# Performance work log

Measured on AMD Instinct MI355X. Metric: run time of the kernel, lower is better.

## Reference

```python
import jax, jax.numpy as jnp
import numpy as np

D_MODEL = 768; N_LAYER = 4; D_STATE = 64; D_CONV = 4; EXPAND = 2; HEADDIM = 64
D_INNER = EXPAND * D_MODEL          # 1536
NHEADS = D_INNER // HEADDIM         # 24
CONV_DIM = D_INNER + 2 * D_STATE    # 1664
D_IN_PROJ = 2 * D_INNER + 2 * D_STATE + NHEADS  # 3224
VOCAB = 50257; EPS = 1e-5


def _ln(x, w, b):
    m = x.mean(-1, keepdims=True)
    v = ((x - m) ** 2).mean(-1, keepdims=True)
    return (x - m) * jax.lax.rsqrt(v + EPS) * w + b


def _silu(x):
    return x * jax.nn.sigmoid(x)


def _mamba2(x, W_in, conv_w, conv_b, dt_bias, A_log, Dp, rms_w, W_out):
    # x: [B, L, d_model]
    Bsz, L, _ = x.shape
    zxbcdt = x @ W_in.T                                   # [B,L,D_IN_PROJ]
    z = zxbcdt[..., :D_INNER]
    xBC = zxbcdt[..., D_INNER:D_INNER + CONV_DIM]
    dt = zxbcdt[..., D_INNER + CONV_DIM:]                 # [B,L,H]
    # causal depthwise conv over time
    xc = jnp.transpose(xBC, (0, 2, 1))                    # [B,C,L]
    xc = jax.lax.conv_general_dilated(
        xc, conv_w[:, None, :], (1,), [(D_CONV - 1, 0)],
        dimension_numbers=('NCH', 'OIH', 'NCH'), feature_group_count=CONV_DIM)
    xBC = _silu(jnp.transpose(xc, (0, 2, 1)) + conv_b)
    xh = xBC[..., :D_INNER].reshape(Bsz, L, NHEADS, HEADDIM)
    Bc = xBC[..., D_INNER:D_INNER + D_STATE]              # [B,L,N]
    Cc = xBC[..., D_INNER + D_STATE:]                     # [B,L,N]
    dt = jax.nn.softplus(dt + dt_bias)                    # [B,L,H]
    dA = jnp.exp(dt * (-jnp.exp(A_log)))                  # [B,L,H]

    def step(h, inp):
        dA_t, dt_t, x_t, B_t, C_t = inp
        h = dA_t[:, :, None, None] * h + (dt_t[:, :, None] * x_t)[..., None] * B_t[:, None, None, :]
        return h, jnp.einsum('bhpn,bn->bhp', h, C_t)

    tm = lambda a: jnp.moveaxis(a, 1, 0)  # time-major
    h0 = jnp.zeros((Bsz, NHEADS, HEADDIM, D_STATE), x.dtype)
    _, y = jax.lax.scan(step, h0, (tm(dA), tm(dt), tm(xh), tm(Bc), tm(Cc)))
    y = jnp.moveaxis(y, 0, 1) + Dp[:, None] * xh          # [B,L,H,P]
    y = y.reshape(Bsz, L, D_INNER) * _silu(z)             # gate
    y = y * jax.lax.rsqrt((y * y).mean(-1, keepdims=True) + EPS) * rms_w
    return y @ W_out.T


def setup_inputs() -> dict:
    key = jax.random.key(0)
    ks = jax.random.split(key, 16)
    B, L = 1, 1024
    idx = jax.random.randint(ks[0], (B, L), 0, VOCAB)
    targets = jax.random.randint(ks[1], (B, L), 0, VOCAB)
    s = 0.02
    emb = jax.random.normal(ks[2], (VOCAB, D_MODEL), jnp.float32) * s
    ln_w = jnp.ones((N_LAYER, D_MODEL)); ln_b = jnp.zeros((N_LAYER, D_MODEL))
    W_in = jax.random.normal(ks[3], (N_LAYER, D_IN_PROJ, D_MODEL), jnp.float32) * s
    conv_w = jax.random.normal(ks[4], (N_LAYER, CONV_DIM, D_CONV), jnp.float32) * 0.1
    conv_b = jnp.zeros((N_LAYER, CONV_DIM))
    dt_bias = jnp.log(jnp.expm1(jax.random.uniform(ks[5], (N_LAYER, NHEADS), minval=0.001, maxval=0.1)))
    A_log = jnp.log(jax.random.uniform(ks[6], (N_LAYER, NHEADS), minval=1.0, maxval=16.0))
    Dp = jnp.ones((N_LAYER, NHEADS))
    rms_w = jnp.ones((N_LAYER, D_INNER))
    W_out = jax.random.normal(ks[7], (N_LAYER, D_MODEL, D_INNER), jnp.float32) * s
    lnf_w = jnp.ones((D_MODEL,)); lnf_b = jnp.zeros((D_MODEL,))
    return {"idx": idx, "targets": targets, "emb": emb, "ln_w": ln_w, "ln_b": ln_b,
            "W_in": W_in, "conv_w": conv_w, "conv_b": conv_b, "dt_bias": dt_bias,
            "A_log": A_log, "Dp": Dp, "rms_w": rms_w, "W_out": W_out,
            "lnf_w": lnf_w, "lnf_b": lnf_b}


def reference(idx, targets, emb, ln_w, ln_b, W_in, conv_w, conv_b, dt_bias,
              A_log, Dp, rms_w, W_out, lnf_w, lnf_b):
    x = emb[idx]                                          # [B,L,D]
    for i in range(N_LAYER):
        x = x + _mamba2(_ln(x, ln_w[i], ln_b[i]), W_in[i], conv_w[i], conv_b[i],
                        dt_bias[i], A_log[i], Dp[i], rms_w[i], W_out[i])
    x = _ln(x, lnf_w, lnf_b)
    logits = x @ emb.T                                    # tied head
    logp = jax.nn.log_softmax(logits, axis=-1)
    loss = -jnp.take_along_axis(logp, targets[..., None], axis=-1).mean()
    return logits, loss
```

## Files before the change

### kernel.cpp

```cpp
#include <hip/hip_runtime.h>
#include <hip/hip_bf16.h>
#include <math.h>

#define SL     1024
#define DMODEL 768
#define NLAYER 4
#define NSTATE 64
#define HEADDIM 64
#define DINNER 1536
#define NHEADS 24
#define CONVDIM 1664
#define DINPROJ 3224
#define VOCABN 50257

typedef __attribute__((ext_vector_type(8))) short short8;
typedef __attribute__((ext_vector_type(4))) short short4v;
typedef __attribute__((ext_vector_type(4))) float f32x4;

__device__ __forceinline__ short f2bf(float f) {
    unsigned int u = __builtin_bit_cast(unsigned int, f);
    u += 0x7fffu + ((u >> 16) & 1u);
    return (short)(u >> 16);
}

#define AS1 __attribute__((address_space(1)))
#define AS3 __attribute__((address_space(3)))
__device__ __forceinline__ void gl2lds16(const void* g, void* l) {
    __builtin_amdgcn_global_load_lds((const AS1 unsigned int*)g,
                                     (AS3 unsigned int*)(unsigned int)(uintptr_t)l,
                                     16, 0, 0);
}

template <int CTRL>
__device__ __forceinline__ float dppadd(float x) {
    int v = __builtin_amdgcn_update_dpp(0, __builtin_bit_cast(int, x), CTRL, 0xf, 0xf, true);
    return x + __builtin_bit_cast(float, v);
}

__global__ void cvt_k(const float* __restrict__ s, short* __restrict__ d, int n) {
    int i = (blockIdx.x * 256 + threadIdx.x) * 4;
    if (i >= n) return;
    float4 v = *(const float4*)(s + i);
    short4v o;
    o.x = f2bf(v.x); o.y = f2bf(v.y); o.z = f2bf(v.z); o.w = f2bf(v.w);
    *(short4v*)(d + i) = o;
}

__global__ void embed_k(const int* __restrict__ idx, const float* __restrict__ emb,
                        float* __restrict__ x) {
    int d = blockIdx.x * 256 + threadIdx.x;
    int t = blockIdx.y;
    x[t * DMODEL + d] = emb[(size_t)idx[t] * DMODEL + d];
}

__global__ void ln_k(const float* __restrict__ x, const float* __restrict__ w,
                     const float* __restrict__ b, short* __restrict__ out) {
    int row = blockIdx.x, t = threadIdx.x;
    const float* xr = x + row * DMODEL;
    float v0 = xr[t], v1 = xr[t + 256], v2 = xr[t + 512];
    float s = v0 + v1 + v2;
    float q = v0 * v0 + v1 * v1 + v2 * v2;
    __shared__ float sa[4], sb[4];
    for (int off = 32; off; off >>= 1) { s += __shfl_down(s, off); q += __shfl_down(q, off); }
    if (!(t & 63)) { sa[t >> 6] = s; sb[t >> 6] = q; }
    __syncthreads();
    s = sa[0] + sa[1] + sa[2] + sa[3];
    q = sb[0] + sb[1] + sb[2] + sb[3];
    float mean = s * (1.f / DMODEL);
    float var  = q * (1.f / DMODEL) - mean * mean;
    float rs = rsqrtf(var + 1e-5f);
    out[row * DMODEL + t      ] = f2bf((v0 - mean) * rs * w[t      ] + b[t      ]);
    out[row * DMODEL + t + 256] = f2bf((v1 - mean) * rs * w[t + 256] + b[t + 256]);
    out[row * DMODEL + t + 512] = f2bf((v2 - mean) * rs * w[t + 512] + b[t + 512]);
}

__global__ __launch_bounds__(512) void gemm_bb_k(const short* __restrict__ A,
                                                 const short* __restrict__ B,
                                                 float* __restrict__ C,
                                                 float2* __restrict__ P,
                                                 int N, int K, int addflag) {
    __shared__ __align__(16) short As[2][16384];
    __shared__ __align__(16) short Bs[2][16384];
    const int t = threadIdx.x;
    const int lane = t & 63, wv = t >> 6;

    const int nwg = gridDim.x;
    int bid = blockIdx.x;
    int qq = nwg >> 3, rr = nwg & 7;
    int xcd = bid & 7, ii = bid >> 3;
    int v = (xcd < rr ? xcd * (qq + 1) : rr * (qq + 1) + (xcd - rr) * qq) + ii;
    const int m0 = (v & 3) * 256;
    const int n0 = (v >> 2) * 256;

    const int wm = (wv >> 2) * 128, wn = (wv & 3) * 64;
    const int q4 = lane >> 4, l16 = lane & 15;

    f32x4 zero4 = {0.f, 0.f, 0.f, 0.f};
    f32x4 acc[8][4];
#pragma unroll
    for (int i = 0; i < 8; i++)
#pragma unroll
        for (int j = 0; j < 4; j++) acc[i][j] = zero4;

    auto stageA = [&](int buf, int kh, int k0) {
#pragma unroll
        for (int i = 0; i < 2; i++) {
            int g = i * 512 + t;
            int q = g >> 8, r = g & 255;
            gl2lds16(A + (size_t)(m0 + r) * K + k0 + kh * 32 + q * 8,
                     &As[buf][kh * 8192 + g * 8]);
        }
    };
    auto stageB = [&](int buf, int kh, int k0) {
#pragma unroll
        for (int i = 0; i < 2; i++) {
            int g = i * 512 + t;
            int q = g >> 8, r = g & 255;
            int gr = n0 + r; if (gr > N - 1) gr = N - 1;
            gl2lds16(B + (size_t)gr * K + k0 + kh * 32 + q * 8,
                     &Bs[buf][kh * 8192 + g * 8]);
        }
    };

    const int NT = K >> 6;
    stageA(0, 0, 0); stageB(0, 0, 0); stageA(0, 1, 0); stageB(0, 1, 0);
    asm volatile("s_waitcnt vmcnt(4)" ::: "memory");
    __builtin_amdgcn_s_barrier();

    for (int tt = 0; tt < NT; tt++) {
        const int cur = tt & 1;
        const bool pf = (tt + 1 < NT);
        const int k1 = (tt + 1) << 6;
        const short* Ac = &As[cur][0];
        const short* Bc = &Bs[cur][0];

        short8 bfk[4];
        {
            short8 af[4];
#pragma unroll
            for (int nt = 0; nt < 4; nt++)
                bfk[nt] = *(const short8*)(Bc + q4 * 2048 + (wn + nt * 16 + l16) * 8);
#pragma unroll
            for (int mt = 0; mt < 4; mt++)
                af[mt] = *(const short8*)(Ac + q4 * 2048 + (wm + mt * 16 + l16) * 8);
            if (pf) stageA(cur ^ 1, 0, k1);
            __builtin_amdgcn_s_barrier();
            __builtin_amdgcn_s_setprio(1);
#pragma unroll
            for (int mt = 0; mt < 4; mt++)
#pragma unroll
                for (int nt = 0; nt < 4; nt++)
                    acc[mt][nt] = __builtin_amdgcn_mfma_f32_16x16x32_bf16(af[mt], bfk[nt], acc[mt][nt], 0, 0, 0);
            __builtin_amdgcn_s_setprio(0);
            __builtin_amdgcn_s_barrier();
        }
        {
            short8 af[4];
#pragma unroll
            for (int mt = 0; mt < 4; mt++)
                af[mt] = *(const short8*)(Ac + q4 * 2048 + (wm + (mt + 4) * 16 + l16) * 8);
            if (pf) stageB(cur ^ 1, 0, k1);
            __builtin_amdgcn_s_barrier();
            __builtin_amdgcn_s_setprio(1);
#pragma unroll
            for (int mt = 0; mt < 4; mt++)
#pragma unroll
                for (int nt = 0; nt < 4; nt++)
                    acc[mt + 4][nt] = __builtin_amdgcn_mfma_f32_16x16x32_bf16(af[mt], bfk[nt], acc[mt + 4][nt], 0, 0, 0);
            __builtin_amdgcn_s_setprio(0);
            if (pf) asm volatile("s_waitcnt vmcnt(4)" ::: "memory");
            else    asm volatile("s_waitcnt vmcnt(0)" ::: "memory");
            __builtin_amdgcn_s_barrier();
        }
        {
            short8 af[4];
#pragma unroll
            for (int nt = 0; nt < 4; nt++)
                bfk[nt] = *(const short8*)(Bc + 8192 + q4 * 2048 + (wn + nt * 16 + l16) * 8);
#pragma unroll
            for (int mt = 0; mt < 4; mt++)
                af[mt] = *(const short8*)(Ac + 8192 + q4 * 2048 + (wm + mt * 16 + l16) * 8);
            if (pf) stageA(cur ^ 1, 1, k1);
            __builtin_amdgcn_s_barrier();
            __builtin_amdgcn_s_setprio(1);
#pragma unroll
            for (int mt = 0; mt < 4; mt++)
#pragma unroll
                for (int nt = 0; nt < 4; nt++)
                    acc[mt][nt] = __builtin_amdgcn_mfma_f32_16x16x32_bf16(af[mt], bfk[nt], acc[mt][nt], 0, 0, 0);
            __builtin_amdgcn_s_setprio(0);
            __builtin_amdgcn_s_barrier();
        }
        {
            short8 af[4];
#pragma unroll
            for (int mt = 0; mt < 4; mt++)
                af[mt] = *(const short8*)(Ac + 8192 + q4 * 2048 + (wm + (mt + 4) * 16 + l16) * 8);
            if (pf) stageB(cur ^ 1, 1, k1);
            __builtin_amdgcn_s_barrier();
            __builtin_amdgcn_s_setprio(1);
#pragma unroll
            for (int mt = 0; mt < 4; mt++)
#pragma unroll
                for (int nt = 0; nt < 4; nt++)
                    acc[mt + 4][nt] = __builtin_amdgcn_mfma_f32_16x16x32_bf16(af[mt], bfk[nt], acc[mt + 4][nt], 0, 0, 0);
            __builtin_amdgcn_s_setprio(0);
            if (pf) asm volatile("s_waitcnt vmcnt(4)" ::: "memory");
            else    asm volatile("s_waitcnt vmcnt(0)" ::: "memory");
            __builtin_amdgcn_s_barrier();
        }
    }

#pragma unroll
    for (int mt = 0; mt < 8; mt++) {
        int row = m0 + wm + mt * 16 + q4 * 4;
#pragma unroll
        for (int nt = 0; nt < 4; nt++) {
            int col = n0 + wn + nt * 16 + l16;
            if (col < N) {
#pragma unroll
                for (int r = 0; r < 4; r++) {
                    size_t o = (size_t)(row + r) * N + col;
                    float val = acc[mt][nt][r];
                    if (addflag) C[o] += val; else C[o] = val;
                }
            }
        }
    }

    float2* lds_ms = (float2*)&As[0][0];
    const int nw = wv & 3;
#pragma unroll
    for (int mt = 0; mt < 8; mt++) {
#pragma unroll
        for (int r = 0; r < 4; r++) {
            float m = -3.0e38f;
#pragma unroll
            for (int nt = 0; nt < 4; nt++) {
                int col = n0 + wn + nt * 16 + l16;
                if (col < N) m = fmaxf(m, acc[mt][nt][r]);
            }
#pragma unroll
            for (int off = 1; off < 16; off <<= 1)
                m = fmaxf(m, __shfl_xor(m, off));
            float s = 0.f;
#pragma unroll
            for (int nt = 0; nt < 4; nt++) {
                int col = n0 + wn + nt * 16 + l16;
                if (col < N) s += __expf(acc[mt][nt][r] - m);
            }
#pragma unroll
            for (int off = 1; off < 16; off <<= 1)
                s += __shfl_xor(s, off);
            if (l16 == 0)
                lds_ms[(wm + mt * 16 + q4 * 4 + r) * 5 + nw] = make_float2(m, s);
        }
    }
    __syncthreads();
    if (t < 256) {
        float m = -3.0e38f, s = 0.f;
#pragma unroll
        for (int w = 0; w < 4; w++) {
            float2 p = lds_ms[t * 5 + w];
            float nm = fmaxf(m, p.x);
            s = s * __expf(m - nm) + p.y * __expf(p.x - nm);
            m = nm;
        }
        P[(size_t)(v >> 2) * 1024 + (m0 + t)] = make_float2(m, s);
    }
}

__global__ __launch_bounds__(256) void gemm64_k(const short* __restrict__ A,
                                                const short* __restrict__ B,
                                                float* __restrict__ C,
                                                int N, int K, int addflag, int nMB) {
    __shared__ __align__(16) short As[2][4096];
    __shared__ __align__(16) short Bs[2][4096];
    const int t = threadIdx.x;
    const int lane = t & 63, wv = t >> 6;

    const int nwg = gridDim.x;
    int bid = blockIdx.x;
    int qq = nwg >> 3, rr = nwg & 7;
    int xcd = bid & 7, ii = bid >> 3;
    int v = (xcd < rr ? xcd * (qq + 1) : rr * (qq + 1) + (xcd - rr) * qq) + ii;
    const int m0 = (v % nMB) * 64, n0 = (v / nMB) * 64;

    const int wm = (wv >> 1) * 32, wn = (wv & 1) * 32;
    const int q4 = lane >> 4, l16 = lane & 15;

    f32x4 zero4 = {0.f, 0.f, 0.f, 0.f};
    f32x4 acc[2][2];
#pragma unroll
    for (int i = 0; i < 2; i++)
#pragma unroll
        for (int j = 0; j < 2; j++) acc[i][j] = zero4;

    auto stage = [&](int buf, int k0) {
#pragma unroll
        for (int i = 0; i < 2; i++) {
            int g = i * 256 + t;
            int q = g >> 6, r = g & 63;
            gl2lds16(A + (size_t)(m0 + r) * K + k0 + q * 8, &As[buf][g * 8]);
        }
#pragma unroll
        for (int i = 0; i < 2; i++) {
            int g = i * 256 + t;
            int q = g >> 6, r = g & 63;
            int gr = n0 + r; if (gr > N - 1) gr = N - 1;
            gl2lds16(B + (size_t)gr * K + k0 + q * 8, &Bs[buf][g * 8]);
        }
    };

    const int NT = K >> 6;
    stage(0, 0);
    for (int tt = 0; tt < NT; tt++) {
        const int cur = tt & 1;
        if (tt + 1 < NT) {
            stage(cur ^ 1, (tt + 1) << 6);
            asm volatile("s_waitcnt vmcnt(4)" ::: "memory");
        } else {
            asm volatile("s_waitcnt vmcnt(0)" ::: "memory");
        }
        __builtin_amdgcn_s_barrier();

        short8 af[2][2], bf[2][2];
#pragma unroll
        for (int kk = 0; kk < 2; kk++) {
#pragma unroll
            for (int mt = 0; mt < 2; mt++)
                af[kk][mt] = *(const short8*)(&As[cur][(kk * 4 + q4) * 512 + (wm + mt * 16 + l16) * 8]);
#pragma unroll
            for (int nt = 0; nt < 2; nt++)
                bf[kk][nt] = *(const short8*)(&Bs[cur][(kk * 4 + q4) * 512 + (wn + nt * 16 + l16) * 8]);
        }
        asm volatile("s_waitcnt lgkmcnt(0)" ::: "memory");
        __builtin_amdgcn_s_barrier();

#pragma unroll
        for (int kk = 0; kk < 2; kk++)
#pragma unroll
            for (int mt = 0; mt < 2; mt++)
#pragma unroll
                for (int nt = 0; nt < 2; nt++)
                    acc[mt][nt] = __builtin_amdgcn_mfma_f32_16x16x32_bf16(af[kk][mt], bf[kk][nt], acc[mt][nt], 0, 0, 0);
    }

#pragma unroll
    for (int mt = 0; mt < 2; mt++) {
        int row = m0 + wm + mt * 16 + (lane >> 4) * 4;
#pragma unroll
        for (int nt = 0; nt < 2; nt++) {
            int col = n0 + wn + nt * 16 + l16;
            if (col < N) {
#pragma unroll
                for (int r = 0; r < 4; r++) {
                    size_t o = (size_t)(row + r) * N + col;
                    float val = acc[mt][nt][r];
                    if (addflag) C[o] += val; else C[o] = val;
                }
            }
        }
    }
}

#define LDSK 56
__global__ __launch_bounds__(256) void gemm_bt_k(const short* __restrict__ A,
                                                 const float* __restrict__ B,
                                                 float* __restrict__ C,
                                                 int N, int K, int addflag) {
    __shared__ __align__(16) short As[128 * LDSK];
    __shared__ __align__(16) short Bs[128 * LDSK];
    const int t = threadIdx.x;
    const int lane = t & 63, wv = t >> 6;
    const int m0 = blockIdx.x * 128, n0 = blockIdx.y * 128;
    const int wm = (wv >> 1) * 64, wn = (wv & 1) * 64;
    f32x4 zero4 = {0.f, 0.f, 0.f, 0.f};
    f32x4 acc[4][4];
#pragma unroll
    for (int i = 0; i < 4; i++)
#pragma unroll
        for (int j = 0; j < 4; j++) acc[i][j] = zero4;
    for (int k0 = 0; k0 < K; k0 += 32) {
        uint4  av[2];
        float4 bv[4];
#pragma unroll
        for (int i = 0; i < 2; i++) {
            int c = i * 256 + t, row = c >> 2, kc = c & 3;
            av[i] = *(const uint4*)(A + (size_t)(m0 + row) * K + k0 + kc * 8);
        }
#pragma unroll
        for (int i = 0; i < 4; i++) {
            int c = i * 256 + t, row = c >> 3, kc = c & 7;
            int gr = n0 + row; if (gr > N - 1) gr = N - 1;
            bv[i] = *(const float4*)(B + (size_t)gr * K + k0 + kc * 4);
        }
        __syncthreads();
#pragma unroll
        for (int i = 0; i < 2; i++) {
            int c = i * 256 + t, row = c >> 2, kc = c & 3;
            *(uint4*)(As + row * LDSK + kc * 8) = av[i];
        }
#pragma unroll
        for (int i = 0; i < 4; i++) {
            int c = i * 256 + t, row = c >> 3, kc = c & 7;
            short4v sv;
            sv.x = f2bf(bv[i].x); sv.y = f2bf(bv[i].y);
            sv.z = f2bf(bv[i].z); sv.w = f2bf(bv[i].w);
            *(short4v*)(Bs + row * LDSK + kc * 4) = sv;
        }
        __syncthreads();
        short8 af[4], bf[4];
#pragma unroll
        for (int mt = 0; mt < 4; mt++)
            af[mt] = *(const short8*)(As + (wm + mt * 16 + (lane & 15)) * LDSK + (lane >> 4) * 8);
#pragma unroll
        for (int nt = 0; nt < 4; nt++)
            bf[nt] = *(const short8*)(Bs + (wn + nt * 16 + (lane & 15)) * LDSK + (lane >> 4) * 8);
#pragma unroll
        for (int mt = 0; mt < 4; mt++)
#pragma unroll
            for (int nt = 0; nt < 4; nt++)
                acc[mt][nt] = __builtin_amdgcn_mfma_f32_16x16x32_bf16(af[mt], bf[nt], acc[mt][nt], 0, 0, 0);
    }
#pragma unroll
    for (int mt = 0; mt < 4; mt++) {
        int row = m0 + wm + mt * 16 + (lane >> 4) * 4;
#pragma unroll
        for (int nt = 0; nt < 4; nt++) {
            int col = n0 + wn + nt * 16 + (lane & 15);
            if (col < N) {
#pragma unroll
                for (int r = 0; r < 4; r++) {
                    size_t o = (size_t)(row + r) * N + col;
                    float val = acc[mt][nt][r];
                    if (addflag) C[o] += val; else C[o] = val;
                }
            }
        }
    }
}

__global__ void convdt_k(const float* __restrict__ zx, const float* __restrict__ cw,
                         const float* __restrict__ cb, const float* __restrict__ dt_bias,
                         const float* __restrict__ A_log, float* __restrict__ xbc,
                         float* __restrict__ dts, float* __restrict__ dAv) {
    int c = blockIdx.x * 256 + threadIdx.x;
    int t = blockIdx.y;
    if (c < CONVDIM) {
        float acc = cb[c];
#pragma unroll
        for (int j = 0; j < 4; j++) {
            int ts = t - 3 + j;
            if (ts >= 0) acc += cw[c * 4 + j] * zx[(size_t)ts * DINPROJ + DINNER + c];
        }
        xbc[(size_t)t * CONVDIM + c] = acc / (1.f + __expf(-acc));
    } else if (c < CONVDIM + NHEADS) {
        int h = c - CONVDIM;
        float d = zx[(size_t)t * DINPROJ + 3200 + h] + dt_bias[h];
        float sp = (d > 20.f) ? d : log1pf(__expf(d));
        dts[t * NHEADS + h] = sp;
        dAv[t * NHEADS + h] = __expf(-__expf(A_log[h]) * sp);
    }
}

__global__ __launch_bounds__(128) void scan_k(const float* __restrict__ xbc,
                                              const float* __restrict__ dts,
                                              const float* __restrict__ dAv,
                                              float* __restrict__ yraw) {
    __shared__ __align__(16) float BCs[64][128];
    __shared__ __align__(16) float xs[64][8];
    __shared__ float dash[64];
    int h = blockIdx.x >> 3;
    int pbase = (blockIdx.x & 7) * 8;
    int t = threadIdx.x, lane = t & 63, wv = t >> 6;
    int pl = wv * 4 + (lane >> 4);
    int n4 = lane & 15;
    float s0 = 0.f, s1 = 0.f, s2 = 0.f, s3 = 0.f;

    for (int tc = 0; tc < 16; tc++) {
        __syncthreads();
#pragma unroll 4
        for (int it = 0; it < 16; it++) {
            int idx = it * 128 + t;
            int trow = idx >> 5, c4 = idx & 31;
            *(float4*)&BCs[trow][c4 * 4] =
                *(const float4*)(xbc + (size_t)(tc * 64 + trow) * CONVDIM + DINNER + c4 * 4);
        }
        {
            int trow = t >> 1, hf = t & 1;
            float dtv = dts[(tc * 64 + trow) * NHEADS + h];
            float4 xv = *(const float4*)(xbc + (size_t)(tc * 64 + trow) * CONVDIM
                                         + h * HEADDIM + pbase + hf * 4);
            xv.x *= dtv; xv.y *= dtv; xv.z *= dtv; xv.w *= dtv;
            *(float4*)&xs[trow][hf * 4] = xv;
        }
        if (t < 64) dash[t] = dAv[(tc * 64 + t) * NHEADS + h];
        __syncthreads();

#pragma unroll 4
        for (int tt = 0; tt < 64; tt++) {
            float4 B4 = *(const float4*)&BCs[tt][n4 * 4];
            float4 C4 = *(const float4*)&BCs[tt][64 + n4 * 4];
            float dtx = xs[tt][pl];
            float da = dash[tt];
            s0 = fmaf(da, s0, dtx * B4.x);
            s1 = fmaf(da, s1, dtx * B4.y);
            s2 = fmaf(da, s2, dtx * B4.z);
            s3 = fmaf(da, s3, dtx * B4.w);
            float part = s0 * C4.x;
            part = fmaf(s1, C4.y, part);
            part = fmaf(s2, C4.z, part);
            part = fmaf(s3, C4.w, part);
            part = dppadd<0xB1>(part);
            part = dppadd<0x4E>(part);
            part = dppadd<0x114>(part);
            part = dppadd<0x118>(part);
            if (n4 == 0)
                yraw[(size_t)(tc * 64 + tt) * DINNER + h * HEADDIM + pbase + pl] = part;
        }
    }
}

__global__ void rms_k(const float* __restrict__ yraw, const float* __restrict__ zx,
                      const float* __restrict__ xbc, const float* __restrict__ Dp,
                      const float* __restrict__ rw, short* __restrict__ yn) {
    int row = blockIdx.x, t = threadIdx.x;
    float v[6];
    float q = 0.f;
#pragma unroll
    for (int j = 0; j < 6; j++) {
        int i = t + j * 256;
        float z  = zx[(size_t)row * DINPROJ + i];
        float xh = xbc[(size_t)row * CONVDIM + i];
        float y  = yraw[(size_t)row * DINNER + i] + Dp[i >> 6] * xh;
        float val = y * (z / (1.f + __expf(-z)));
        v[j] = val;
        q += val * val;
    }
    __shared__ float sb[4];
    for (int off = 32; off; off >>= 1) q += __shfl_down(q, off);
    if (!(t & 63)) sb[t >> 6] = q;
    __syncthreads();
    q = sb[0] + sb[1] + sb[2] + sb[3];
    float rs = rsqrtf(q * (1.f / DINNER) + 1e-5f);
#pragma unroll
    for (int j = 0; j < 6; j++) {
        int i = t + j * 256;
        yn[(size_t)row * DINNER + i] = f2bf(v[j] * rs * rw[i]);
    }
}

__global__ void loss_row_k(const float* __restrict__ logits, const int* __restrict__ tg,
                           float* __restrict__ lossp) {
    int r = blockIdx.x, t = threadIdx.x;
    const float* lr = logits + (size_t)r * VOCABN;
    float m = -3.0e38f, s = 0.f;
    for (int j = t; j < VOCABN; j += 256) {
        float v = lr[j];
        if (v > m) { s = s * __expf(m - v) + 1.f; m = v; }
        else s += __expf(v - m);
    }
    for (int off = 32; off; off >>= 1) {
        float mo = __shfl_down(m, off), so = __shfl_down(s, off);
        float nm = fmaxf(m, mo);
        s = s * __expf(m - nm) + so * __expf(mo - nm);
        m = nm;
    }
    __shared__ float sm[4], ss[4];
    if (!(t & 63)) { sm[t >> 6] = m; ss[t >> 6] = s; }
    __syncthreads();
    if (t == 0) {
        m = sm[0]; s = ss[0];
        for (int w = 1; w < 4; w++) {
            float nm = fmaxf(m, sm[w]);
            s = s * __expf(m - nm) + ss[w] * __expf(sm[w] - nm);
            m = nm;
        }
        lossp[r] = (m + logf(s)) - lr[tg[r]];
    }
}

__global__ void loss_fin2_k(const float2* __restrict__ P, const float* __restrict__ logits,
                            const int* __restrict__ tg, float* __restrict__ lossp) {
    int r = blockIdx.x * 256 + threadIdx.x;
    float m = -3.0e38f, s = 0.f;
    for (int p = 0; p < 197; p++) {
        float2 q = P[(size_t)p * 1024 + r];
        float nm = fmaxf(m, q.x);
        s = s * __expf(m - nm) + q.y * __expf(q.x - nm);
        m = nm;
    }
    lossp[r] = (m + logf(s)) - logits[(size_t)r * VOCABN + tg[r]];
}

__global__ void loss_fin_k(const float* __restrict__ lossp, float* __restrict__ out) {
    int t = threadIdx.x;
    float s = lossp[t] + lossp[t + 256] + lossp[t + 512] + lossp[t + 768];
    for (int off = 32; off; off >>= 1) s += __shfl_down(s, off);
    __shared__ float sb[4];
    if (!(t & 63)) sb[t >> 6] = s;
    __syncthreads();
    if (t == 0) out[(size_t)SL * VOCABN] = (sb[0] + sb[1] + sb[2] + sb[3]) * (1.f / SL);
}

extern "C" void kernel_launch(void* const* d_in, const int* in_sizes, int n_in,
                              void* d_out, int out_size, void* d_ws, size_t ws_size,
                              hipStream_t stream) {
    const int*   idx     = (const int*)d_in[0];
    const int*   targets = (const int*)d_in[1];
    const float* emb     = (const float*)d_in[2];
    const float* ln_w    = (const float*)d_in[3];
    const float* ln_b    = (const float*)d_in[4];
    const float* W_in    = (const float*)d_in[5];
    const float* conv_w  = (const float*)d_in[6];
    const float* conv_b  = (const float*)d_in[7];
    const float* dt_bias = (const float*)d_in[8];
    const float* A_log   = (const float*)d_in[9];
    const float* Dp      = (const float*)d_in[10];
    const float* rms_w   = (const float*)d_in[11];
    const float* W_out   = (const float*)d_in[12];
    const float* lnf_w   = (const float*)d_in[13];
    const float* lnf_b   = (const float*)d_in[14];

    char* ws = (char*)d_ws;
    float* x     = (float*)(ws + 0);
    short* xn    = (short*)(ws + 3145728);
    float* zx    = (float*)(ws + 4718592);
    float* xbc   = (float*)(ws + 17924096);
    float* dts   = (float*)(ws + 24739840);
    float* dAv   = (float*)(ws + 24838144);
    float* yraw  = (float*)(ws + 24936448);
    short* yn    = (short*)(ws + 31227904);
    float* lossp = (float*)(ws + 34373632);
    short* wInb  = (short*)(ws + 34377728);
    short* wOutb = (short*)(ws + 54183936);
    short* embb  = (short*)(ws + 63621120);
    float2* pms  = (float2*)(ws + 4718592);
    float* logits = (float*)d_out;

    const bool big = ws_size >= 140815872ull;

    if (big) {
        int nWin  = NLAYER * DINPROJ * DMODEL;
        int nWout = NLAYER * DMODEL * DINNER;
        int nEmb  = VOCABN * DMODEL;
        cvt_k<<<(nWin / 4 + 255) / 256, 256, 0, stream>>>(W_in, wInb, nWin);
        cvt_k<<<(nWout / 4 + 255) / 256, 256, 0, stream>>>(W_out, wOutb, nWout);
        cvt_k<<<(nEmb / 4 + 255) / 256, 256, 0, stream>>>(emb, embb, nEmb);
    }

    embed_k<<<dim3(3, SL), 256, 0, stream>>>(idx, emb, x);
    for (int l = 0; l < NLAYER; l++) {
        ln_k<<<SL, 256, 0, stream>>>(x, ln_w + l * DMODEL, ln_b + l * DMODEL, xn);
        if (big)
            gemm64_k<<<816, 256, 0, stream>>>(xn, wInb + (size_t)l * DINPROJ * DMODEL,
                                              zx, DINPROJ, DMODEL, 0, 16);
        else
            gemm_bt_k<<<dim3(8, 26), 256, 0, stream>>>(xn, W_in + (size_t)l * DINPROJ * DMODEL,
                                                       zx, DINPROJ, DMODEL, 0);
        convdt_k<<<dim3(7, SL), 256, 0, stream>>>(zx, conv_w + l * CONVDIM * 4,
                                                  conv_b + l * CONVDIM,
                                                  dt_bias + l * NHEADS, A_log + l * NHEADS,
                                                  xbc, dts, dAv);
        scan_k<<<192, 128, 0, stream>>>(xbc, dts, dAv, yraw);
        rms_k<<<SL, 256, 0, stream>>>(yraw, zx, xbc, Dp + l * NHEADS, rms_w + l * DINNER, yn);
        if (big)
            gemm64_k<<<192, 256, 0, stream>>>(yn, wOutb + (size_t)l * DMODEL * DINNER,
                                              x, DMODEL, DINNER, 1, 16);
        else
            gemm_bt_k<<<dim3(8, 6), 256, 0, stream>>>(yn, W_out + (size_t)l * DMODEL * DINNER,
                                                      x, DMODEL, DINNER, 1);
    }
    ln_k<<<SL, 256, 0, stream>>>(x, lnf_w, lnf_b, xn);
    if (big) {
        gemm_bb_k<<<4 * 197, 512, 0, stream>>>(xn, embb, logits, pms, VOCABN, DMODEL, 0);
        loss_fin2_k<<<4, 256, 0, stream>>>(pms, logits, targets, lossp);
    } else {
        gemm_bt_k<<<dim3(8, 393), 256, 0, stream>>>(xn, emb, logits, VOCABN, DMODEL, 0);
        loss_row_k<<<SL, 256, 0, stream>>>(logits, targets, lossp);
    }
    loss_fin_k<<<1, 256, 0, stream>>>(lossp, logits);
}
```

Baseline: 1.123 ms.

## Split scan state dimension across two waves and use two-pass max in loss finalize

The selective-scan kernel now runs 256 threads per block instead of 128. Each half of the waves handles 32 of the 64 state entries, so each thread keeps two running states instead of four. The two partial outputs are combined through shared memory and written back in a coalesced pass, which adds an extra barrier per time chunk. Separately, the loss finalize kernel first takes the max over all partials and then sums the exponentials, replacing the online rescaling at the cost of reading the partials twice.

Result: faster. 1.046 ms (-6.9%).

```diff
diff --git a/kernel.cpp b/kernel.cpp
--- a/kernel.cpp
+++ b/kernel.cpp
@@ -464,30 +464,33 @@
     }
 }
 
-__global__ __launch_bounds__(128) void scan_k(const float* __restrict__ xbc,
+__global__ __launch_bounds__(256) void scan_k(const float* __restrict__ xbc,
                                               const float* __restrict__ dts,
                                               const float* __restrict__ dAv,
                                               float* __restrict__ yraw) {
     __shared__ __align__(16) float BCs[64][128];
     __shared__ __align__(16) float xs[64][8];
     __shared__ float dash[64];
+    __shared__ float ys[64][8][2];
     int h = blockIdx.x >> 3;
     int pbase = (blockIdx.x & 7) * 8;
     int t = threadIdx.x, lane = t & 63, wv = t >> 6;
-    int pl = wv * 4 + (lane >> 4);
+    int nh = wv >> 1;
+    int pl = (wv & 1) * 4 + (lane >> 4);
     int n4 = lane & 15;
-    float s0 = 0.f, s1 = 0.f, s2 = 0.f, s3 = 0.f;
+    int nbase = nh * 32;
+    float s0 = 0.f, s1 = 0.f;
 
     for (int tc = 0; tc < 16; tc++) {
         __syncthreads();
 #pragma unroll 4
-        for (int it = 0; it < 16; it++) {
-            int idx = it * 128 + t;
+        for (int it = 0; it < 8; it++) {
+            int idx = it * 256 + t;
             int trow = idx >> 5, c4 = idx & 31;
             *(float4*)&BCs[trow][c4 * 4] =
                 *(const float4*)(xbc + (size_t)(tc * 64 + trow) * CONVDIM + DINNER + c4 * 4);
         }
-        {
+        if (t < 128) {
             int trow = t >> 1, hf = t & 1;
             float dtv = dts[(tc * 64 + trow) * NHEADS + h];
             float4 xv = *(const float4*)(xbc + (size_t)(tc * 64 + trow) * CONVDIM
@@ -500,24 +503,27 @@
 
 #pragma unroll 4
         for (int tt = 0; tt < 64; tt++) {
-            float4 B4 = *(const float4*)&BCs[tt][n4 * 4];
-            float4 C4 = *(const float4*)&BCs[tt][64 + n4 * 4];
+            float2 B2 = *(const float2*)&BCs[tt][nbase + n4 * 2];
+            float2 C2 = *(const float2*)&BCs[tt][64 + nbase + n4 * 2];
             float dtx = xs[tt][pl];
             float da = dash[tt];
-            s0 = fmaf(da, s0, dtx * B4.x);
-            s1 = fmaf(da, s1, dtx * B4.y);
-            s2 = fmaf(da, s2, dtx * B4.z);
-            s3 = fmaf(da, s3, dtx * B4.w);
-            float part = s0 * C4.x;
-            part = fmaf(s1, C4.y, part);
-            part = fmaf(s2, C4.z, part);
-            part = fmaf(s3, C4.w, part);
+            s0 = fmaf(da, s0, dtx * B2.x);
+            s1 = fmaf(da, s1, dtx * B2.y);
+            float part = s0 * C2.x;
+            part = fmaf(s1, C2.y, part);
             part = dppadd<0xB1>(part);
             part = dppadd<0x4E>(part);
             part = dppadd<0x114>(part);
             part = dppadd<0x118>(part);
-            if (n4 == 0)
-                yraw[(size_t)(tc * 64 + tt) * DINNER + h * HEADDIM + pbase + pl] = part;
+            if (n4 == 0) ys[tt][pl][nh] = part;
+        }
+        __syncthreads();
+#pragma unroll
+        for (int i = 0; i < 2; i++) {
+            int idx = i * 256 + t;
+            int tt2 = idx >> 3, pl2 = idx & 7;
+            float yv = ys[tt2][pl2][0] + ys[tt2][pl2][1];
+            yraw[(size_t)(tc * 64 + tt2) * DINNER + h * HEADDIM + pbase + pl2] = yv;
         }
     }
 }
@@ -584,12 +590,13 @@
 __global__ void loss_fin2_k(const float2* __restrict__ P, const float* __restrict__ logits,
                             const int* __restrict__ tg, float* __restrict__ lossp) {
     int r = blockIdx.x * 256 + threadIdx.x;
-    float m = -3.0e38f, s = 0.f;
+    float m = -3.0e38f;
+    for (int p = 0; p < 197; p++)
+        m = fmaxf(m, P[(size_t)p * 1024 + r].x);
+    float s = 0.f;
     for (int p = 0; p < 197; p++) {
         float2 q = P[(size_t)p * 1024 + r];
-        float nm = fmaxf(m, q.x);
-        s = s * __expf(m - nm) + q.y * __expf(q.x - nm);
-        m = nm;
+        s += q.y * __expf(q.x - m);
     }
     lossp[r] = (m + logf(s)) - logits[(size_t)r * VOCABN + tg[r]];
 }
@@ -663,7 +670,7 @@
                                                   conv_b + l * CONVDIM,
                                                   dt_bias + l * NHEADS, A_log + l * NHEADS,
                                                   xbc, dts, dAv);
-        scan_k<<<192, 128, 0, stream>>>(xbc, dts, dAv, yraw);
+        scan_k<<<192, 256, 0, stream>>>(xbc, dts, dAv, yraw);
         rms_k<<<SL, 256, 0, stream>>>(yraw, zx, xbc, Dp + l * NHEADS, rms_w + l * DINNER, yn);
         if (big)
             gemm64_k<<<192, 256, 0, stream>>>(yn, wOutb + (size_t)l * DMODEL * DINNER,
```
